# Kernel tuning notes

Measured on AMD Instinct MI355X. Metric: run time of the kernel, lower is better.

Reference implementation:

```python
import jax, jax.numpy as jnp
from jax import lax
import numpy as np

NUM_HEADS = 16
NUM_HEADS_KV = 4
HEAD_DIM = 128
D_CONV = 4
ROT_DIM = 128
ROT_BASE = 10000.0
CAUSAL = True


def setup_inputs() -> dict:
    key = jax.random.key(0)
    ks = jax.random.split(key, 7)
    B, S, E = 2, 2048, 2048
    QKV = HEAD_DIM * (NUM_HEADS + 2 * NUM_HEADS_KV)  # 3072
    return {
        "x": jax.random.normal(ks[0], (B, S, E), jnp.float32),
        "W_in": jax.random.normal(ks[1], (QKV, E), jnp.float32) * 0.02,
        "b_in": jax.random.normal(ks[2], (QKV,), jnp.float32) * 0.02,
        "conv_w": jax.random.normal(ks[3], (QKV, D_CONV), jnp.float32) * 0.1,
        "conv_b": jax.random.normal(ks[4], (QKV,), jnp.float32) * 0.02,
        "W_out": jax.random.normal(ks[5], (E, NUM_HEADS * HEAD_DIM), jnp.float32) * 0.02,
        "b_out": jax.random.normal(ks[6], (E,), jnp.float32) * 0.02,
    }


def _rotary(x, cos, sin):
    # x: [B,S,H,D], non-interleaved rotary over first ROT_DIM dims (here full D)
    x1, x2 = x[..., : ROT_DIM // 2], x[..., ROT_DIM // 2 : ROT_DIM]
    c = cos[None, :, None, :]
    s = sin[None, :, None, :]
    rot = jnp.concatenate([x1 * c - x2 * s, x2 * c + x1 * s], axis=-1)
    return jnp.concatenate([rot, x[..., ROT_DIM:]], axis=-1)


def reference(x, W_in, b_in, conv_w, conv_b, W_out, b_out):
    B, S, E = x.shape
    QKV = conv_w.shape[0]
    # fused in-projection
    qkv = jnp.einsum("bse,fe->bsf", x, W_in) + b_in  # [B,S,QKV]
    # depthwise causal conv1d (left pad d_conv-1, equivalent to torch pad+trim)
    qkv_t = jnp.transpose(qkv, (0, 2, 1))  # [B,C,S]
    qkv_t = jnp.pad(qkv_t, ((0, 0), (0, 0), (D_CONV - 1, 0)))
    conv = lax.conv_general_dilated(
        qkv_t, conv_w[:, None, :], window_strides=(1,), padding="VALID",
        feature_group_count=QKV, dimension_numbers=("NCH", "OIH", "NCH"))
    qkv = jnp.transpose(conv + conv_b[None, :, None], (0, 2, 1))  # [B,S,QKV]
    # split q / kv
    q_dim = NUM_HEADS * HEAD_DIM
    q = qkv[..., :q_dim].reshape(B, S, NUM_HEADS, HEAD_DIM)
    kv = qkv[..., q_dim:].reshape(B, S, 2, NUM_HEADS_KV, HEAD_DIM)
    k, v = kv[:, :, 0], kv[:, :, 1]
    # rotary embedding on q and k
    t = jnp.arange(S, dtype=jnp.float32)
    inv_freq = 1.0 / (ROT_BASE ** (jnp.arange(0, ROT_DIM, 2, dtype=jnp.float32) / ROT_DIM))
    freqs = t[:, None] * inv_freq[None, :]  # [S, ROT_DIM/2]
    cos, sin = jnp.cos(freqs), jnp.sin(freqs)
    q = _rotary(q, cos, sin)
    k = _rotary(k, cos, sin)
    # GQA: repeat kv heads
    rep = NUM_HEADS // NUM_HEADS_KV
    k = jnp.repeat(k, rep, axis=2)  # [B,S,H,D]
    v = jnp.repeat(v, rep, axis=2)
    scale = 1.0 / jnp.sqrt(jnp.float32(HEAD_DIM))
    scores = jnp.einsum("bshd,bthd->bhst", q, k) * scale  # [B,H,S,S]
    if CAUSAL:
        mask = jnp.tril(jnp.ones((S, S), dtype=bool))
        scores = jnp.where(mask[None, None], scores, jnp.finfo(scores.dtype).min)
    attn = jax.nn.softmax(scores, axis=-1)
    ctx = jnp.einsum("bhst,bthd->bshd", attn, v).reshape(B, S, q_dim)
    return jnp.einsum("bsf,ef->bse", ctx, W_out) + b_out
```

## Files before the change

kernel.cpp:

```cpp
#include <hip/hip_runtime.h>
#include <hip/hip_bf16.h>

#define B_   2
#define S_   2048
#define E_   2048
#define QKV_ 3072
#define NH   16
#define NKV  4
#define HD   128
#define SL   16

typedef __attribute__((ext_vector_type(8))) short bf16x8;
typedef __attribute__((ext_vector_type(4))) float f32x4;
typedef unsigned short u16;
typedef unsigned int   u32;

__device__ __forceinline__ float bf2f(u16 u) {
  union { u32 i; float f; } v; v.i = ((u32)u) << 16; return v.f;
}
__device__ __forceinline__ u16 f2bf(float f) {
  union { float f; u32 u; } v; v.f = f;
  return (u16)((v.u + 0x7FFFu + ((v.u >> 16) & 1u)) >> 16);
}
__device__ __forceinline__ u32 pkbf(float a, float b) {
  __hip_bfloat162 h = __float22bfloat162_rn(float2{a, b});
  u32 r; __builtin_memcpy(&r, &h, 4); return r;
}
__device__ __forceinline__ float ex2(float x) { return __builtin_amdgcn_exp2f(x); }
__device__ __forceinline__ void load_lds16(const u16* g, u16* l) {
  __builtin_amdgcn_global_load_lds((const __attribute__((address_space(1))) void*)g,
                                   (__attribute__((address_space(3))) void*)l, 16, 0, 0);
}

__global__ __launch_bounds__(256) void f2b_conv(const float* __restrict__ in,
                                                u16* __restrict__ out, int n4) {
  const int i = blockIdx.x * 256 + threadIdx.x;
  if (i >= n4) return;
  const float4 v = ((const float4*)in)[i];
  ushort4 o;
  o.x = f2bf(v.x); o.y = f2bf(v.y); o.z = f2bf(v.z); o.w = f2bf(v.w);
  ((ushort4*)out)[i] = o;
}

__global__ __launch_bounds__(256) void rope_tab(float* __restrict__ c,
                                                float* __restrict__ s) {
  const int idx = blockIdx.x * 256 + threadIdx.x;
  const int t = idx >> 6, i = idx & 63;
  const float invf = powf(10000.0f, -(float)i * (1.0f / 64.0f));
  float sn, cs;
  sincosf((float)t * invf, &sn, &cs);
  c[idx] = cs; s[idx] = sn;
}

template <int OUT_BF16>
__global__ __launch_bounds__(256) void gemm_bt(const u16* __restrict__ A,
                                               const u16* __restrict__ Bm,
                                               const float* __restrict__ bias,
                                               void* __restrict__ C,
                                               int M, int N, int K) {
  __shared__ u16 As[128 * 32];
  __shared__ u16 Bs[128 * 32];
  const int tid = threadIdx.x;
  const int wave = tid >> 6, lane = tid & 63;
  const int m0 = blockIdx.y * 128, n0 = blockIdx.x * 128;
  const int wm = (wave & 1) * 64, wn = (wave >> 1) * 64;
  const int L15 = lane & 15, Lq = lane >> 4;
  const int lrow = lane >> 2, lcol = (lane & 3) * 8;

  f32x4 acc[4][4] = {};

  for (int k0 = 0; k0 < K; k0 += 32) {
#pragma unroll
    for (int c = 0; c < 2; ++c) {
      const int chunk = c * 4 + wave;
      const int row = chunk * 16 + lrow;
      load_lds16(A  + (size_t)(m0 + row) * K + k0 + lcol, &As[chunk * 512 + lane * 8]);
      load_lds16(Bm + (size_t)(n0 + row) * K + k0 + lcol, &Bs[chunk * 512 + lane * 8]);
    }
    __syncthreads();
    bf16x8 af[4], bfr[4];
#pragma unroll
    for (int t = 0; t < 4; ++t) {
      af[t]  = *(const bf16x8*)&As[(wm + t * 16 + L15) * 32 + Lq * 8];
      bfr[t] = *(const bf16x8*)&Bs[(wn + t * 16 + L15) * 32 + Lq * 8];
    }
#pragma unroll
    for (int mt = 0; mt < 4; ++mt)
#pragma unroll
      for (int nt = 0; nt < 4; ++nt)
        acc[mt][nt] = __builtin_amdgcn_mfma_f32_16x16x32_bf16(af[mt], bfr[nt], acc[mt][nt], 0, 0, 0);
    __syncthreads();
  }

#pragma unroll
  for (int nt = 0; nt < 4; ++nt) {
    const int col = n0 + wn + nt * 16 + L15;
    const float bv = bias[col];
#pragma unroll
    for (int mt = 0; mt < 4; ++mt) {
#pragma unroll
      for (int r = 0; r < 4; ++r) {
        const int row = m0 + wm + mt * 16 + Lq * 4 + r;
        const float v = acc[mt][nt][r] + bv;
        if (OUT_BF16) ((u16*)C)[(size_t)row * N + col] = f2bf(v);
        else          ((float*)C)[(size_t)row * N + col] = v;
      }
    }
  }
}

__global__ __launch_bounds__(256) void conv_rope(const u16* __restrict__ qkv,
                                                 const float* __restrict__ cw,
                                                 const float* __restrict__ cb,
                                                 const float* __restrict__ ct,
                                                 const float* __restrict__ st,
                                                 u16* __restrict__ qo,
                                                 u16* __restrict__ ko,
                                                 u16* __restrict__ vtmp) {
  const int blk = blockIdx.x;
  const int b = blk >> 7;
  const int s0 = (blk & 127) * SL;
  const u16* qb = qkv + (size_t)b * S_ * QKV_;

  for (int u = threadIdx.x; u < 896; u += 256) {
    if (u < 640) {
      const int hs = u >> 5, ip = u & 31, i = ip * 2;
      int f1; u16* outbase; float scale;
      if (hs < 16) {
        f1 = hs * HD + i;
        outbase = qo + (size_t)(b * NH + hs) * S_ * HD;
        scale = 0.08838834764831845f * 1.4426950408889634f;
      } else {
        f1 = NH * HD + (hs - 16) * HD + i;
        outbase = ko + (size_t)(b * NKV + (hs - 16)) * S_ * HD;
        scale = 1.0f;
      }
      const int f2 = f1 + 64;
      const float4 wA0 = *(const float4*)&cw[f1 * 4];
      const float4 wA1 = *(const float4*)&cw[(f1 + 1) * 4];
      const float4 wB0 = *(const float4*)&cw[f2 * 4];
      const float4 wB1 = *(const float4*)&cw[(f2 + 1) * 4];
      const float cA0 = cb[f1], cA1 = cb[f1 + 1], cB0 = cb[f2], cB1 = cb[f2 + 1];
      float A0[3], A1[3], B0[3], B1[3];
#pragma unroll
      for (int j = 0; j < 3; ++j) {
        const int t = s0 - 3 + j;
        if (t >= 0) {
          const u32 pa = *(const u32*)&qb[(size_t)t * QKV_ + f1];
          const u32 pb = *(const u32*)&qb[(size_t)t * QKV_ + f2];
          A0[j] = bf2f((u16)pa); A1[j] = bf2f((u16)(pa >> 16));
          B0[j] = bf2f((u16)pb); B1[j] = bf2f((u16)(pb >> 16));
        } else { A0[j] = A1[j] = B0[j] = B1[j] = 0.f; }
      }
      for (int s = s0; s < s0 + SL; ++s) {
        const u32 pa = *(const u32*)&qb[(size_t)s * QKV_ + f1];
        const u32 pb = *(const u32*)&qb[(size_t)s * QKV_ + f2];
        const float nA0 = bf2f((u16)pa), nA1 = bf2f((u16)(pa >> 16));
        const float nB0 = bf2f((u16)pb), nB1 = bf2f((u16)(pb >> 16));
        const float x1a = cA0 + wA0.x * A0[0] + wA0.y * A0[1] + wA0.z * A0[2] + wA0.w * nA0;
        const float x1b = cA1 + wA1.x * A1[0] + wA1.y * A1[1] + wA1.z * A1[2] + wA1.w * nA1;
        const float x2a = cB0 + wB0.x * B0[0] + wB0.y * B0[1] + wB0.z * B0[2] + wB0.w * nB0;
        const float x2b = cB1 + wB1.x * B1[0] + wB1.y * B1[1] + wB1.z * B1[2] + wB1.w * nB1;
        const float2 cs = *(const float2*)&ct[s * 64 + i];
        const float2 sn = *(const float2*)&st[s * 64 + i];
        u16* outp = outbase + (size_t)s * HD;
        *(u32*)&outp[i]      = pkbf((x1a * cs.x - x2a * sn.x) * scale,
                                    (x1b * cs.y - x2b * sn.y) * scale);
        *(u32*)&outp[i + 64] = pkbf((x2a * cs.x + x1a * sn.x) * scale,
                                    (x2b * cs.y + x1b * sn.y) * scale);
        A0[0] = A0[1]; A0[1] = A0[2]; A0[2] = nA0;
        A1[0] = A1[1]; A1[1] = A1[2]; A1[2] = nA1;
        B0[0] = B0[1]; B0[1] = B0[2]; B0[2] = nB0;
        B1[0] = B1[1]; B1[1] = B1[2]; B1[2] = nB1;
      }
    } else {
      const int vu = u - 640, h = vu >> 6, d = (vu & 63) * 2;
      const int f = (NH + NKV) * HD + h * HD + d;
      const float4 w0 = *(const float4*)&cw[f * 4];
      const float4 w1 = *(const float4*)&cw[(f + 1) * 4];
      const float c0 = cb[f], c1 = cb[f + 1];
      float V0[3], V1[3];
#pragma unroll
      for (int j = 0; j < 3; ++j) {
        const int t = s0 - 3 + j;
        if (t >= 0) {
          const u32 p = *(const u32*)&qb[(size_t)t * QKV_ + f];
          V0[j] = bf2f((u16)p); V1[j] = bf2f((u16)(p >> 16));
        } else { V0[j] = V1[j] = 0.f; }
      }
      u16* vrow = vtmp + (size_t)(b * NKV + h) * S_ * HD + d;
      for (int s = s0; s < s0 + SL; ++s) {
        const u32 p = *(const u32*)&qb[(size_t)s * QKV_ + f];
        const float n0 = bf2f((u16)p), n1 = bf2f((u16)(p >> 16));
        const float v0 = c0 + w0.x * V0[0] + w0.y * V0[1] + w0.z * V0[2] + w0.w * n0;
        const float v1 = c1 + w1.x * V1[0] + w1.y * V1[1] + w1.z * V1[2] + w1.w * n1;
        *(u32*)&vrow[(size_t)s * HD] = pkbf(v0, v1);
        V0[0] = V0[1]; V0[1] = V0[2]; V0[2] = n0;
        V1[0] = V1[1]; V1[1] = V1[2]; V1[2] = n1;
      }
    }
  }
}

__global__ __launch_bounds__(256) void vtrans(const u16* __restrict__ vin,
                                              u16* __restrict__ vout) {
  __shared__ u16 t[64][72];
  const int bh = blockIdx.z;
  const int d0 = blockIdx.y * 64;
  const int s0 = blockIdx.x * 64;
  const u16* ip = vin + ((size_t)bh * S_ + s0) * HD + d0;
  const int r = threadIdx.x >> 4, c4 = (threadIdx.x & 15) * 4;
#pragma unroll
  for (int j = 0; j < 4; ++j) {
    const ushort4 v = *(const ushort4*)&ip[(size_t)(r + j * 16) * HD + c4];
    t[c4 + 0][r + j * 16] = v.x;
    t[c4 + 1][r + j * 16] = v.y;
    t[c4 + 2][r + j * 16] = v.z;
    t[c4 + 3][r + j * 16] = v.w;
  }
  __syncthreads();
  const int dl = threadIdx.x >> 2, sc = (threadIdx.x & 3) * 16;
  u16* op = vout + (size_t)bh * HD * S_ + (size_t)(d0 + dl) * S_ + s0 + sc;
  *(bf16x8*)op       = *(const bf16x8*)&t[dl][sc];
  *(bf16x8*)(op + 8) = *(const bf16x8*)&t[dl][sc + 8];
}

__global__ __launch_bounds__(256, 2) void attn(const u16* __restrict__ q,
                                               const u16* __restrict__ k,
                                               const u16* __restrict__ v,
                                               u16* __restrict__ ctx) {
  __shared__ u16 Ks[2][64 * 128];
  __shared__ u16 Vs[128 * 64];
  __shared__ u16 P[4][16 * 64];
  const int tid = threadIdx.x, wave = tid >> 6, lane = tid & 63;
  const int L15 = lane & 15, Lq = lane >> 4;
  const int bh = blockIdx.y;
  const int b = bh >> 4, h = bh & 15, hk = h >> 2;

  const u16* kb = k + (size_t)(b * NKV + hk) * S_ * HD;
  const u16* vb = v + (size_t)(b * NKV + hk) * HD * S_;

  const int rx = L15 & 7;
  int koff[4], voff[2], poff[2];
#pragma unroll
  for (int c = 0; c < 4; ++c) koff[c] = ((c * 4 + Lq) ^ rx) * 8;
#pragma unroll
  for (int kc = 0; kc < 2; ++kc) {
    voff[kc] = ((kc * 4 + Lq) ^ rx) * 8;
    poff[kc] = L15 * 64 + ((kc * 4 + Lq) ^ rx) * 8;
  }

  const int ksl = tid >> 4, kcp = tid & 15;
  const int vsl = tid >> 3, vcp = tid & 7;

  for (int pass = 0; pass < 2; ++pass) {
    const int qt = pass ? (31 - blockIdx.x) : blockIdx.x;
    const int q0 = qt * 64;
    const int base = q0 + wave * 16;

    bf16x8 qf[4];
    {
      const u16* qp = q + ((size_t)bh * S_ + base + L15) * HD + Lq * 8;
#pragma unroll
      for (int c = 0; c < 4; ++c) qf[c] = *(const bf16x8*)(qp + c * 32);
    }

    f32x4 acc[8] = {};
    float m_i[4], l_i[4];
#pragma unroll
    for (int r = 0; r < 4; ++r) { m_i[r] = -1e30f; l_i[r] = 0.f; }

    const int ktmax = qt + 1;

#pragma unroll
    for (int j = 0; j < 4; ++j) {
      const int krow = j * 16 + ksl;
      load_lds16(kb + (size_t)krow * HD + (kcp ^ (krow & 7)) * 8,
                 &Ks[0][(krow * 16 + kcp) * 8]);
      const int vrow = j * 32 + vsl;
      load_lds16(vb + (size_t)vrow * S_ + (vcp ^ (vrow & 7)) * 8,
                 &Vs[(vrow * 8 + vcp) * 8]);
    }
    __syncthreads();

    for (int kt = 0; kt < ktmax; ++kt) {
      const int k0 = kt * 64;
      const int cur = kt & 1;
      if (kt > 0) {
#pragma unroll
        for (int j = 0; j < 4; ++j) {
          const int vrow = j * 32 + vsl;
          load_lds16(vb + (size_t)vrow * S_ + k0 + (vcp ^ (vrow & 7)) * 8,
                     &Vs[(vrow * 8 + vcp) * 8]);
        }
      }
      if (kt + 1 < ktmax) {
        const int kn = k0 + 64;
#pragma unroll
        for (int j = 0; j < 4; ++j) {
          const int krow = j * 16 + ksl;
          load_lds16(kb + (size_t)(kn + krow) * HD + (kcp ^ (krow & 7)) * 8,
                     &Ks[cur ^ 1][(krow * 16 + kcp) * 8]);
        }
      }
      f32x4 sc[4];
#pragma unroll
      for (int nt = 0; nt < 4; ++nt) sc[nt] = f32x4{0.f, 0.f, 0.f, 0.f};
#pragma unroll
      for (int nt = 0; nt < 4; ++nt) {
#pragma unroll
        for (int c = 0; c < 4; ++c) {
          const bf16x8 kf = *(const bf16x8*)&Ks[cur][(nt * 16 + L15) * 128 + koff[c]];
          sc[nt] = __builtin_amdgcn_mfma_f32_16x16x32_bf16(qf[c], kf, sc[nt], 0, 0, 0);
        }
      }
      if (k0 + 63 > base) {
#pragma unroll
        for (int nt = 0; nt < 4; ++nt) {
          const int col = k0 + nt * 16 + L15;
#pragma unroll
          for (int r = 0; r < 4; ++r) {
            const int row = base + Lq * 4 + r;
            if (col > row) sc[nt][r] = -1e30f;
          }
        }
      }
      float mloc[4];
      bool nm = false;
#pragma unroll
      for (int r = 0; r < 4; ++r) {
        float m = fmaxf(fmaxf(sc[0][r], sc[1][r]), fmaxf(sc[2][r], sc[3][r]));
        m = fmaxf(m, __shfl_xor(m, 1));
        m = fmaxf(m, __shfl_xor(m, 2));
        m = fmaxf(m, __shfl_xor(m, 4));
        m = fmaxf(m, __shfl_xor(m, 8));
        mloc[r] = m;
        nm |= (m > m_i[r]);
      }
      const bool anynew = (__ballot(nm) != 0ull);
      float rsum[4];
      {
        float mnew[4];
#pragma unroll
        for (int r = 0; r < 4; ++r) {
          mnew[r] = anynew ? fmaxf(m_i[r], mloc[r]) : m_i[r];
          rsum[r] = 0.f;
        }
        float pv[4][4];
#pragma unroll
        for (int nt = 0; nt < 4; ++nt)
#pragma unroll
          for (int r = 0; r < 4; ++r) {
            pv[nt][r] = ex2(sc[nt][r] - mnew[r]);
            rsum[r] += pv[nt][r];
          }
#pragma unroll
        for (int nt = 0; nt < 4; ++nt) {
          const int cch = nt * 2 + (L15 >> 3), clo = L15 & 7;
#pragma unroll
          for (int rp = 0; rp < 2; ++rp) {
            const u32 pk = pkbf(pv[nt][rp * 2], pv[nt][rp * 2 + 1]);
            const int row0 = Lq * 4 + rp * 2;
            P[wave][row0 * 64 + (((cch ^ (row0 & 7)) << 3) | clo)] = (u16)pk;
            const int row1 = row0 + 1;
            P[wave][row1 * 64 + (((cch ^ (row1 & 7)) << 3) | clo)] = (u16)(pk >> 16);
          }
        }
        if (anynew) {
          float alpha[4];
#pragma unroll
          for (int r = 0; r < 4; ++r) {
            alpha[r] = ex2(m_i[r] - mnew[r]);
            m_i[r] = mnew[r];
          }
#pragma unroll
          for (int dt = 0; dt < 8; ++dt)
#pragma unroll
            for (int r = 0; r < 4; ++r) acc[dt][r] *= alpha[r];
#pragma unroll
          for (int r = 0; r < 4; ++r) l_i[r] *= alpha[r];
        }
      }
#pragma unroll
      for (int r = 0; r < 4; ++r) {
        float s = rsum[r];
        s += __shfl_xor(s, 1);
        s += __shfl_xor(s, 2);
        s += __shfl_xor(s, 4);
        s += __shfl_xor(s, 8);
        l_i[r] += s;
      }
      __syncthreads();
      {
        bf16x8 pa[2];
#pragma unroll
        for (int kc = 0; kc < 2; ++kc)
          pa[kc] = *(const bf16x8*)&P[wave][poff[kc]];
#pragma unroll
        for (int dt = 0; dt < 8; ++dt)
#pragma unroll
          for (int kc = 0; kc < 2; ++kc) {
            const bf16x8 vf = *(const bf16x8*)&Vs[(dt * 16 + L15) * 64 + voff[kc]];
            acc[dt] = __builtin_amdgcn_mfma_f32_16x16x32_bf16(pa[kc], vf, acc[dt], 0, 0, 0);
          }
      }
      __syncthreads();
    }
    {
      float inv[4];
#pragma unroll
      for (int r = 0; r < 4; ++r) inv[r] = 1.f / l_i[r];
      u16* cp = ctx + ((size_t)b * S_ + base) * (NH * HD) + h * HD;
#pragma unroll
      for (int dt = 0; dt < 8; ++dt)
#pragma unroll
        for (int rp = 0; rp < 2; ++rp) {
          const u32 pk = pkbf(acc[dt][rp * 2] * inv[rp * 2],
                              acc[dt][rp * 2 + 1] * inv[rp * 2 + 1]);
          cp[(size_t)(Lq * 4 + rp * 2) * (NH * HD) + dt * 16 + L15] = (u16)pk;
          cp[(size_t)(Lq * 4 + rp * 2 + 1) * (NH * HD) + dt * 16 + L15] = (u16)(pk >> 16);
        }
    }
  }
}

extern "C" void kernel_launch(void* const* d_in, const int* in_sizes, int n_in,
                              void* d_out, int out_size, void* d_ws, size_t ws_size,
                              hipStream_t stream) {
  const float* x     = (const float*)d_in[0];
  const float* W_in  = (const float*)d_in[1];
  const float* b_in  = (const float*)d_in[2];
  const float* cw    = (const float*)d_in[3];
  const float* cb    = (const float*)d_in[4];
  const float* W_out = (const float*)d_in[5];
  const float* b_out = (const float*)d_in[6];

  char* ws = (char*)d_ws;
  u16* xb   = (u16*)(ws);
  u16* wib  = (u16*)(ws + 16777216);
  u16* wob  = (u16*)(ws + 29360128);
  u16* qkv  = (u16*)(ws + 37748736);
  u16* q_ws = (u16*)(ws + 62914560);
  u16* k_ws = (u16*)(ws + 79691776);
  u16* vt_ws= (u16*)(ws + 83886080);
  float* ctab = (float*)ws;
  float* stab = (float*)(ws + 524288);
  u16* vtmp = wib;
  u16* ctx  = xb;

  const int nx = B_ * S_ * E_ / 4, nwi = QKV_ * E_ / 4, nwo = E_ * NH * HD / 4;
  f2b_conv<<<dim3((nx  + 255) / 256), 256, 0, stream>>>(x,     xb,  nx);
  f2b_conv<<<dim3((nwi + 255) / 256), 256, 0, stream>>>(W_in,  wib, nwi);
  f2b_conv<<<dim3((nwo + 255) / 256), 256, 0, stream>>>(W_out, wob, nwo);

  gemm_bt<1><<<dim3(QKV_ / 128, (B_ * S_) / 128), 256, 0, stream>>>(
      xb, wib, b_in, (void*)qkv, B_ * S_, QKV_, E_);
  rope_tab<<<dim3(S_ * 64 / 256), 256, 0, stream>>>(ctab, stab);
  conv_rope<<<dim3(B_ * (S_ / SL)), 256, 0, stream>>>(qkv, cw, cb, ctab, stab, q_ws, k_ws, vtmp);
  vtrans<<<dim3(S_ / 64, HD / 64, B_ * NKV), 256, 0, stream>>>(vtmp, vt_ws);
  attn<<<dim3(16, B_ * NH), 256, 0, stream>>>(q_ws, k_ws, vt_ws, ctx);
  gemm_bt<0><<<dim3(E_ / 128, (B_ * S_) / 128), 256, 0, stream>>>(
      ctx, wob, b_out, d_out, B_ * S_, E_, NH * HD);
}
```

Before: 361.0 us.

## Replace GEMM with 256x256 double-buffered, XOR-swizzled, pipelined MFMA kernel

Replaces the 128x128 single-buffered GEMM (K-step 32, sync per step) with a 512-thread 256x256 tile kernel using K-step 64. Shared memory is double-buffered and XOR-swizzled. Global-to-LDS loads for the next tiles are interleaved between four MFMA quadrants, with explicit vmcnt waits and barriers, and setprio is raised around the MFMA bursts. The aim is to hide memory latency, cut LDS bank conflicts and raise data reuse in both projection GEMMs. In exchange it uses 128KB of LDS and many accumulator registers, and the grid becomes smaller (e.g. 12x16 and 8x16 blocks), which may leave CUs underused.

```diff
diff --git a/kernel.cpp b/kernel.cpp
--- a/kernel.cpp
+++ b/kernel.cpp
@@ -53,60 +53,134 @@
 }
 
 template <int OUT_BF16>
-__global__ __launch_bounds__(256) void gemm_bt(const u16* __restrict__ A,
-                                               const u16* __restrict__ Bm,
-                                               const float* __restrict__ bias,
-                                               void* __restrict__ C,
-                                               int M, int N, int K) {
-  __shared__ u16 As[128 * 32];
-  __shared__ u16 Bs[128 * 32];
+__global__ __launch_bounds__(512, 2) void gemm256(const u16* __restrict__ A,
+                                                  const u16* __restrict__ Bm,
+                                                  const float* __restrict__ bias,
+                                                  void* __restrict__ C,
+                                                  int M, int N, int K) {
+  __shared__ u16 sm[2][2][256 * 64];
   const int tid = threadIdx.x;
-  const int wave = tid >> 6, lane = tid & 63;
-  const int m0 = blockIdx.y * 128, n0 = blockIdx.x * 128;
-  const int wm = (wave & 1) * 64, wn = (wave >> 1) * 64;
+  const int lane = tid & 63;
+  const int wave = tid >> 6;
+  const int wm = wave >> 2, wn = wave & 3;
   const int L15 = lane & 15, Lq = lane >> 4;
-  const int lrow = lane >> 2, lcol = (lane & 3) * 8;
-
-  f32x4 acc[4][4] = {};
-
-  for (int k0 = 0; k0 < K; k0 += 32) {
-#pragma unroll
-    for (int c = 0; c < 2; ++c) {
-      const int chunk = c * 4 + wave;
-      const int row = chunk * 16 + lrow;
-      load_lds16(A  + (size_t)(m0 + row) * K + k0 + lcol, &As[chunk * 512 + lane * 8]);
-      load_lds16(Bm + (size_t)(n0 + row) * K + k0 + lcol, &Bs[chunk * 512 + lane * 8]);
-    }
-    __syncthreads();
-    bf16x8 af[4], bfr[4];
-#pragma unroll
-    for (int t = 0; t < 4; ++t) {
-      af[t]  = *(const bf16x8*)&As[(wm + t * 16 + L15) * 32 + Lq * 8];
-      bfr[t] = *(const bf16x8*)&Bs[(wn + t * 16 + L15) * 32 + Lq * 8];
-    }
-#pragma unroll
-    for (int mt = 0; mt < 4; ++mt)
-#pragma unroll
-      for (int nt = 0; nt < 4; ++nt)
-        acc[mt][nt] = __builtin_amdgcn_mfma_f32_16x16x32_bf16(af[mt], bfr[nt], acc[mt][nt], 0, 0, 0);
-    __syncthreads();
+  const int m0 = blockIdx.y * 256, n0 = blockIdx.x * 256;
+  const int NT = K >> 6;
+
+  const int srow = tid >> 3;
+  const int sdst = (tid & 7) * 8;
+  const int ssrc = ((tid & 7) ^ (srow & 7)) * 8;
+
+  auto stageA = [&](int T, int h, int j) {
+    const int row = h * 128 + j * 64 + srow;
+    load_lds16(A + (size_t)(m0 + row) * K + T * 64 + ssrc,
+               &sm[T & 1][0][row * 64 + sdst]);
+  };
+  auto stageB = [&](int T, int h, int j) {
+    const int row = h * 128 + j * 64 + srow;
+    load_lds16(Bm + (size_t)(n0 + row) * K + T * 64 + ssrc,
+               &sm[T & 1][1][row * 64 + sdst]);
+  };
+  auto rdA = [&](int p, int ms, int mf, int kk) -> bf16x8 {
+    const int row = wm * 128 + ms * 64 + mf * 16 + L15;
+    const int u = (kk * 4 + Lq) ^ (row & 7);
+    return *(const bf16x8*)&sm[p][0][row * 64 + u * 8];
+  };
+  auto rdB = [&](int p, int ns, int nf, int kk) -> bf16x8 {
+    const int row = wn * 64 + ns * 32 + nf * 16 + L15;
+    const int u = (kk * 4 + Lq) ^ (row & 7);
+    return *(const bf16x8*)&sm[p][1][row * 64 + u * 8];
+  };
+
+  f32x4 acc[8][4] = {};
+
+  stageA(0, 0, 0); stageA(0, 0, 1);
+  stageB(0, 0, 0); stageB(0, 0, 1);
+  stageA(0, 1, 0); stageA(0, 1, 1);
+  stageB(0, 1, 0); stageB(0, 1, 1);
+  stageB(1, 0, 0); stageB(1, 0, 1);
+  stageA(1, 0, 0); stageA(1, 0, 1);
+  asm volatile("s_waitcnt vmcnt(4)" ::: "memory");
+  asm volatile("s_barrier" ::: "memory");
+
+  bf16x8 af[4][2], bf0[2][2], bf1[2][2];
+
+#define MFMA_QUAD(MS, NS, BF)                                                     \
+  __builtin_amdgcn_s_setprio(1);                                                  \
+  __builtin_amdgcn_sched_barrier(0);                                              \
+  _Pragma("unroll")                                                               \
+  for (int kk = 0; kk < 2; ++kk)                                                  \
+    _Pragma("unroll")                                                             \
+    for (int mf = 0; mf < 4; ++mf)                                                \
+      _Pragma("unroll")                                                           \
+      for (int nf = 0; nf < 2; ++nf)                                              \
+        acc[MS * 4 + mf][NS * 2 + nf] = __builtin_amdgcn_mfma_f32_16x16x32_bf16(  \
+            af[mf][kk], BF[nf][kk], acc[MS * 4 + mf][NS * 2 + nf], 0, 0, 0);      \
+  __builtin_amdgcn_sched_barrier(0);                                              \
+  __builtin_amdgcn_s_setprio(0);
+
+  for (int T = 0; T < NT; ++T) {
+    const int p = T & 1;
+#pragma unroll
+    for (int mf = 0; mf < 4; ++mf)
+#pragma unroll
+      for (int kk = 0; kk < 2; ++kk) af[mf][kk] = rdA(p, 0, mf, kk);
+#pragma unroll
+    for (int nf = 0; nf < 2; ++nf)
+#pragma unroll
+      for (int kk = 0; kk < 2; ++kk) bf0[nf][kk] = rdB(p, 0, nf, kk);
+    if (T + 1 < NT) { stageA(T + 1, 1, 0); stageA(T + 1, 1, 1); }
+    asm volatile("s_barrier" ::: "memory");
+    MFMA_QUAD(0, 0, bf0)
+    asm volatile("s_barrier" ::: "memory");
+#pragma unroll
+    for (int nf = 0; nf < 2; ++nf)
+#pragma unroll
+      for (int kk = 0; kk < 2; ++kk) bf1[nf][kk] = rdB(p, 1, nf, kk);
+    if (T + 1 < NT) { stageB(T + 1, 1, 0); stageB(T + 1, 1, 1); }
+    asm volatile("s_barrier" ::: "memory");
+    MFMA_QUAD(0, 1, bf1)
+    asm volatile("s_barrier" ::: "memory");
+#pragma unroll
+    for (int mf = 0; mf < 4; ++mf)
+#pragma unroll
+      for (int kk = 0; kk < 2; ++kk) af[mf][kk] = rdA(p, 1, mf, kk);
+    if (T + 2 < NT) { stageB(T + 2, 0, 0); stageB(T + 2, 0, 1); }
+    asm volatile("s_barrier" ::: "memory");
+    MFMA_QUAD(1, 0, bf0)
+    asm volatile("s_barrier" ::: "memory");
+    if (T + 2 < NT) {
+      stageA(T + 2, 0, 0); stageA(T + 2, 0, 1);
+      asm volatile("s_waitcnt vmcnt(4)" ::: "memory");
+    } else {
+      asm volatile("s_waitcnt vmcnt(0)" ::: "memory");
+    }
+    asm volatile("s_barrier" ::: "memory");
+    MFMA_QUAD(1, 1, bf1)
+    asm volatile("s_barrier" ::: "memory");
   }
-
-#pragma unroll
-  for (int nt = 0; nt < 4; ++nt) {
-    const int col = n0 + wn + nt * 16 + L15;
-    const float bv = bias[col];
-#pragma unroll
-    for (int mt = 0; mt < 4; ++mt) {
-#pragma unroll
-      for (int r = 0; r < 4; ++r) {
-        const int row = m0 + wm + mt * 16 + Lq * 4 + r;
-        const float v = acc[mt][nt][r] + bv;
-        if (OUT_BF16) ((u16*)C)[(size_t)row * N + col] = f2bf(v);
-        else          ((float*)C)[(size_t)row * N + col] = v;
-      }
-    }
-  }
+#undef MFMA_QUAD
+
+#pragma unroll
+  for (int ms = 0; ms < 2; ++ms)
+#pragma unroll
+    for (int mf = 0; mf < 4; ++mf) {
+      const int grow0 = m0 + wm * 128 + ms * 64 + mf * 16 + Lq * 4;
+#pragma unroll
+      for (int ns = 0; ns < 2; ++ns)
+#pragma unroll
+        for (int nf = 0; nf < 2; ++nf) {
+          const int gcol = n0 + wn * 64 + ns * 32 + nf * 16 + L15;
+          const float bv = bias[gcol];
+          const f32x4 v = acc[ms * 4 + mf][ns * 2 + nf];
+#pragma unroll
+          for (int r = 0; r < 4; ++r) {
+            const float o = v[r] + bv;
+            if (OUT_BF16) ((u16*)C)[(size_t)(grow0 + r) * N + gcol] = f2bf(o);
+            else          ((float*)C)[(size_t)(grow0 + r) * N + gcol] = o;
+          }
+        }
+    }
 }
 
 __global__ __launch_bounds__(256) void conv_rope(const u16* __restrict__ qkv,
@@ -453,12 +527,12 @@
   f2b_conv<<<dim3((nwi + 255) / 256), 256, 0, stream>>>(W_in,  wib, nwi);
   f2b_conv<<<dim3((nwo + 255) / 256), 256, 0, stream>>>(W_out, wob, nwo);
 
-  gemm_bt<1><<<dim3(QKV_ / 128, (B_ * S_) / 128), 256, 0, stream>>>(
+  gemm256<1><<<dim3(QKV_ / 256, (B_ * S_) / 256), 512, 0, stream>>>(
       xb, wib, b_in, (void*)qkv, B_ * S_, QKV_, E_);
   rope_tab<<<dim3(S_ * 64 / 256), 256, 0, stream>>>(ctab, stab);
   conv_rope<<<dim3(B_ * (S_ / SL)), 256, 0, stream>>>(qkv, cw, cb, ctab, stab, q_ws, k_ws, vtmp);
   vtrans<<<dim3(S_ / 64, HD / 64, B_ * NKV), 256, 0, stream>>>(vtmp, vt_ws);
   attn<<<dim3(16, B_ * NH), 256, 0, stream>>>(q_ws, k_ws, vt_ws, ctx);
-  gemm_bt<0><<<dim3(E_ / 128, (B_ * S_) / 128), 256, 0, stream>>>(
+  gemm256<0><<<dim3(E_ / 256, (B_ * S_) / 256), 512, 0, stream>>>(
       ctx, wob, b_out, d_out, B_ * S_, E_, NH * HD);
 }
```

Measured after the change: 356.3 us. About the same (-1.3%).
